# Performance work log

Measured on AMD Instinct MI355X. Metric: run time of the kernel, lower is better.

Reference implementation:

```python
import jax, jax.numpy as jnp
import numpy as np

K_MASK = -2.3819763e+38
ROPE_THETA = 1000000
MROPE_SECTION = (24, 20, 20)
NORM_EPS = 1e-6


def rms_norm(x, w, eps=NORM_EPS):
    dtype = x.dtype
    x32 = x.astype(jnp.float32)
    rms_inv = jax.lax.rsqrt(jnp.mean(x32 * x32, axis=-1, keepdims=True) + eps)
    return w * (x32 * rms_inv).astype(dtype)


def apply_rope(inputs, positions, head_dim, rope_theta=ROPE_THETA, mrope_section=MROPE_SECTION):
    # positions: [3, B, T] (temporal, height, width); inputs: [B, T, heads, head_dim]
    fraction = 2 * jnp.arange(0, head_dim // 2, dtype=jnp.float32) / head_dim
    timescale = rope_theta ** fraction  # [head_dim//2]
    sinusoid = positions[:, :, :, None].astype(jnp.float32) / timescale  # [3,B,T,hd/2]
    freq = sinusoid[0]
    h_idx = jnp.arange(1, mrope_section[1] * 3, 3)
    w_idx = jnp.arange(2, mrope_section[2] * 3, 3)
    freq = freq.at[..., h_idx].set(sinusoid[1][..., h_idx])
    freq = freq.at[..., w_idx].set(sinusoid[2][..., w_idx])
    freq = freq[:, :, None, :]  # [B,T,1,hd/2]
    sin, cos = jnp.sin(freq), jnp.cos(freq)
    first, second = jnp.split(inputs, 2, axis=-1)
    out = jnp.concatenate([first * cos - second * sin, second * cos + first * sin], axis=-1)
    return out.astype(inputs.dtype)


def setup_inputs() -> dict:
    key = jax.random.key(0)
    ks = jax.random.split(key, 6)
    B, T, D, N, K, H = 2, 1024, 2560, 32, 8, 128
    x = jax.random.normal(ks[0], (B, T, D), dtype=jnp.float32)
    positions = jnp.broadcast_to(jnp.arange(T, dtype=jnp.int32), (3, B, T))
    attn_mask = jnp.tril(jnp.ones((T, T), dtype=bool))[None].repeat(B, axis=0)  # causal [B,T,T]
    wq = jax.random.normal(ks[1], (D, N, H), dtype=jnp.float32) * 0.02
    wk = jax.random.normal(ks[2], (D, K, H), dtype=jnp.float32) * 0.02
    wv = jax.random.normal(ks[3], (D, K, H), dtype=jnp.float32) * 0.02
    wo = jax.random.normal(ks[4], (N, H, D), dtype=jnp.float32) * 0.02
    q_norm_w = jnp.ones((H,), dtype=jnp.float32)
    k_norm_w = jnp.ones((H,), dtype=jnp.float32)
    return {"x": x, "positions": positions, "attn_mask": attn_mask, "wq": wq,
            "wk": wk, "wv": wv, "wo": wo, "q_norm_w": q_norm_w, "k_norm_w": k_norm_w}


def reference(x, positions, attn_mask, wq, wk, wv, wo, q_norm_w, k_norm_w):
    head_dim = wo.shape[1]
    scale = head_dim ** -0.5
    q = rms_norm(jnp.einsum('btd,dnh->btnh', x, wq), q_norm_w)
    k = rms_norm(jnp.einsum('bsd,dkh->bskh', x, wk), k_norm_w)
    v = jnp.einsum('bsd,dkh->bskh', x, wv)
    q = apply_rope(q, positions, head_dim)
    k = apply_rope(k, positions, head_dim)
    b, t, qh, d = q.shape
    _, s, kh, _ = k.shape
    q = q.reshape((b, t, kh, qh // kh, d))  # GQA grouping
    attn = jnp.einsum('bthgd,bshd->bhgts', q, k) * scale
    attn = attn.reshape((b, qh, t, s))
    attn = jnp.where(attn_mask[:, None, :, :], attn, K_MASK)
    attn = jax.nn.softmax(attn.astype(jnp.float32), axis=-1).astype(k.dtype)
    attn = attn.reshape((b, kh, qh // kh, t, s))
    qkv = jnp.einsum('bhgts,bshd->bthgd', attn, v).reshape((b, t, qh, d))
    return jnp.einsum('btnh,nhd->btd', qkv, wo)
```

## Files before the change

kernel.cpp:

```cpp
#include <hip/hip_runtime.h>
#include <hip/hip_bf16.h>

typedef __attribute__((ext_vector_type(8))) __bf16 bf8_t;
typedef __attribute__((ext_vector_type(4))) float f32x4;
typedef __attribute__((ext_vector_type(16))) float f32x16;

#define GLOAD16(gptr, lptr)                                                              \
  __builtin_amdgcn_global_load_lds((const __attribute__((address_space(1))) void*)(gptr), \
                                   (__attribute__((address_space(3))) void*)(lptr), 16, 0, 0)

__device__ __forceinline__ unsigned short f2bf(float f) {
  union { float f; unsigned u; } v; v.f = f;
  return (unsigned short)((v.u + 0x7fffu + ((v.u >> 16) & 1u)) >> 16);
}

__device__ __forceinline__ float bf2f(unsigned short u) {
  union { unsigned u; float f; } v; v.u = ((unsigned)u) << 16;
  return v.f;
}

__device__ __forceinline__ unsigned cvtpk_bf16(float a, float b) {
  unsigned r;
  asm("v_cvt_pk_bf16_f32 %0, %1, %2" : "=v"(r) : "v"(a), "v"(b));
  return r;
}

__global__ void cast_bf16(const float* __restrict__ in, unsigned short* __restrict__ out, int n4) {
  int i = blockIdx.x * blockDim.x + threadIdx.x;
  if (i >= n4) return;
  float4 v = ((const float4*)in)[i];
  ushort4 o;
  o.x = f2bf(v.x); o.y = f2bf(v.y); o.z = f2bf(v.z); o.w = f2bf(v.w);
  ((ushort4*)out)[i] = o;
}

__global__ void tcast(const float* __restrict__ in, unsigned short* __restrict__ out,
                      int R, int C, int ld, int rowOff) {
  __shared__ float tile[32][33];
  int c0 = blockIdx.x * 32, r0 = blockIdx.y * 32;
  int tx = threadIdx.x, ty = threadIdx.y;
#pragma unroll
  for (int i = 0; i < 4; ++i)
    tile[ty + 8 * i][tx] = in[(size_t)(r0 + ty + 8 * i) * C + c0 + tx];
  __syncthreads();
#pragma unroll
  for (int i = 0; i < 4; ++i)
    out[(size_t)(rowOff + c0 + ty + 8 * i) * ld + r0 + tx] = f2bf(tile[tx][ty + 8 * i]);
}

__global__ __launch_bounds__(512, 2) void gemm256(
    const unsigned short* __restrict__ A,
    const unsigned short* __restrict__ Bt,
    float* __restrict__ C0, float* __restrict__ C1,
    unsigned short* __restrict__ Cb,
    int N, int ldk, int Kslice, int nTileN) {
  __shared__ unsigned short SM[4][2][8192];
  int ks = blockIdx.y;
  int kbase = ks * Kslice;
  int nwg = gridDim.x;
  int bidx = blockIdx.x;
  int wg = ((bidx & 7) * (nwg >> 3)) + (bidx >> 3);
  int bm = wg / nTileN, bn = wg % nTileN;
  int m0 = bm << 8, n0 = bn << 8;
  int tid = threadIdx.x, lane = tid & 63, w = tid >> 6;
  int wm = w >> 2, wn = w & 3;
  int lrow = lane & 15, lch = lane >> 4;
  int srow = tid >> 2;
  int scol = ((tid & 3) ^ ((srow >> 1) & 3)) << 3;
  int nt = Kslice >> 5;

  f32x4 acc[8][4] = {};

  auto stage = [&](int t) {
    int buf = t & 3;
    int k0 = kbase + (t << 5);
    const unsigned short* Ag = A + (size_t)(m0 + srow) * ldk + k0 + scol;
    const unsigned short* Bg = Bt + (size_t)(n0 + srow) * ldk + k0 + scol;
    unsigned short* Al = &SM[buf][0][w << 9];
    unsigned short* Bl = &SM[buf][1][w << 9];
    GLOAD16(Ag, Al);
    GLOAD16(Ag + (size_t)128 * ldk, Al + 4096);
    GLOAD16(Bg, Bl);
    GLOAD16(Bg + (size_t)128 * ldk, Bl + 4096);
  };

  stage(0);
  stage(1);
  stage(2);
  for (int t = 0; t < nt; ++t) {
    if (t + 2 < nt)      asm volatile("s_waitcnt vmcnt(8)" ::: "memory");
    else if (t + 1 < nt) asm volatile("s_waitcnt vmcnt(4)" ::: "memory");
    else                 asm volatile("s_waitcnt vmcnt(0)" ::: "memory");
    asm volatile("s_barrier" ::: "memory");
    if (t + 3 < nt) stage(t + 3);
    int buf = t & 3;
    const unsigned short* As = &SM[buf][0][0];
    const unsigned short* Bs = &SM[buf][1][0];
    bf8_t a[8], b[4];
#pragma unroll
    for (int mi = 0; mi < 8; ++mi) {
      int ar = (wm << 7) + (mi << 4) + lrow;
      a[mi] = *(const bf8_t*)(As + ar * 32 + ((lch ^ ((ar >> 1) & 3)) << 3));
    }
#pragma unroll
    for (int ni = 0; ni < 4; ++ni) {
      int br = (wn << 6) + (ni << 4) + lrow;
      b[ni] = *(const bf8_t*)(Bs + br * 32 + ((lch ^ ((br >> 1) & 3)) << 3));
    }
    __builtin_amdgcn_s_setprio(1);
#pragma unroll
    for (int mi = 0; mi < 8; ++mi)
#pragma unroll
      for (int ni = 0; ni < 4; ++ni)
        acc[mi][ni] = __builtin_amdgcn_mfma_f32_16x16x32_bf16(a[mi], b[ni], acc[mi][ni], 0, 0, 0);
    __builtin_amdgcn_s_setprio(0);
  }
  int r0 = m0 + (wm << 7) + (lch << 2);
  int c0 = n0 + (wn << 6) + lrow;
  if (Cb) {
#pragma unroll
    for (int mi = 0; mi < 8; ++mi)
#pragma unroll
      for (int ni = 0; ni < 4; ++ni)
#pragma unroll
        for (int r = 0; r < 4; ++r)
          Cb[(size_t)(r0 + (mi << 4) + r) * N + c0 + (ni << 4)] = f2bf(acc[mi][ni][r]);
  } else {
    float* __restrict__ C = ks ? C1 : C0;
#pragma unroll
    for (int mi = 0; mi < 8; ++mi)
#pragma unroll
      for (int ni = 0; ni < 4; ++ni)
#pragma unroll
        for (int r = 0; r < 4; ++r)
          C[(size_t)(r0 + (mi << 4) + r) * N + c0 + (ni << 4)] = acc[mi][ni][r];
  }
}

__global__ void reduce_add(const float4* __restrict__ a, const float4* __restrict__ b,
                           float4* __restrict__ o, int n4) {
  int i = blockIdx.x * blockDim.x + threadIdx.x;
  if (i >= n4) return;
  float4 x = a[i], y = b[i];
  o[i] = make_float4(x.x + y.x, x.y + y.y, x.z + y.z, x.w + y.w);
}

__global__ __launch_bounds__(128) void normrope(
    const unsigned short* __restrict__ qkv, const int* __restrict__ positions,
    const float* __restrict__ qw, const float* __restrict__ kw,
    unsigned short* __restrict__ qb, unsigned short* __restrict__ kb,
    unsigned short* __restrict__ vt) {
  int blk = blockIdx.x;
  int hh = blk % 48, bt = blk / 48;
  int b = bt >> 10, t = bt & 1023;
  int tid = threadIdx.x;
  int colbase = (hh < 32) ? (hh << 7) : ((hh < 40) ? (4096 + ((hh - 32) << 7)) : (5120 + ((hh - 40) << 7)));
  float val = bf2f(qkv[(size_t)bt * 6144 + colbase + tid]);
  if (hh >= 40) {
    vt[((size_t)((b * 8 + hh - 40) * 128 + tid)) * 1024 + t] = f2bf(val);
    return;
  }
  __shared__ float red[2];
  __shared__ float xs[128];
  float ss = val * val;
#pragma unroll
  for (int m = 32; m >= 1; m >>= 1) ss += __shfl_xor(ss, m);
  if ((tid & 63) == 0) red[tid >> 6] = ss;
  __syncthreads();
  float rinv = rsqrtf((red[0] + red[1]) * (1.0f / 128.0f) + 1e-6f);
  float wgt = (hh < 32) ? qw[tid] : kw[tid];
  float xn = val * rinv * wgt;
  xs[tid] = xn;
  __syncthreads();
  float other = xs[tid ^ 64];
  int pos = positions[b * 1024 + t];
  int j = tid & 63;
  float ang = (float)pos * exp2f(-(float)j * 0.31143075889569027f);
  float sv = sinf(ang), cv = cosf(ang);
  float outv = (tid < 64) ? (xn * cv - other * sv) : (xn * cv + other * sv);
  if (hh >= 32) outv *= 0.12751744f;
  unsigned short o = f2bf(outv);
  if (hh < 32) qb[((size_t)((b * 32 + hh) * 1024 + t)) * 128 + tid] = o;
  else kb[((size_t)((b * 8 + hh - 32) * 1024 + t)) * 128 + tid] = o;
}

__global__ __launch_bounds__(256, 2) void attn(
    const unsigned short* __restrict__ qb,
    const unsigned short* __restrict__ kb,
    const unsigned short* __restrict__ vt,
    unsigned short* __restrict__ ob) {
  __shared__ unsigned short Kl[2][64 * 128];
  __shared__ unsigned short Vl[2][128 * 64];
  int bx = blockIdx.x, hq = blockIdx.y, b = blockIdx.z;
  int qt = (bx < 4) ? (7 - bx) : (bx - 4);
  int kvh = hq >> 2;
  int tid = threadIdx.x, lane = tid & 63, w = tid >> 6;
  int qlane = lane & 31, h = lane >> 5;
  int q0 = (qt << 7) + (w << 5);
  int qg = q0 + qlane;
  const unsigned short* kbase = kb + ((size_t)(b * 8 + kvh) << 17);
  const unsigned short* vbase = vt + ((size_t)(b * 8 + kvh) << 17);

  const unsigned short* qptr = qb + ((size_t)((b * 32 + hq) * 1024 + qg) << 7) + (h << 3);
  bf8_t qf[8];
#pragma unroll
  for (int ds = 0; ds < 8; ++ds) qf[ds] = *(const bf8_t*)(qptr + ds * 16);

  f32x16 o[4] = {};
  float mrun = -3.0e38f, lrun = 0.f;
  int last_st = (q0 + 31) >> 6;
  int nsteps = 2 * qt + 2;

  auto stage = [&](int st, int buf) {
    int s0 = st << 6;
    unsigned short* kd = &Kl[buf][0];
    unsigned short* vd = &Vl[buf][0];
#pragma unroll
    for (int i = 0; i < 4; ++i) {
      int cid = i * 256 + tid;
      int kr = cid >> 4, ksl = cid & 15;
      GLOAD16(kbase + (size_t)(s0 + kr) * 128 + ((ksl ^ (kr & 15)) << 3), kd + cid * 8);
      int vr = cid >> 3, vsl = cid & 7;
      GLOAD16(vbase + (size_t)vr * 1024 + s0 + ((vsl ^ (vr & 7)) << 3), vd + cid * 8);
    }
  };

  stage(0, 0);
  for (int st = 0; st < nsteps; ++st) {
    __syncthreads();
    if (st + 1 < nsteps) stage(st + 1, (st + 1) & 1);
    if (st <= last_st) {
      const char* Kb = (const char*)&Kl[st & 1][0];
      const char* Vb = (const char*)&Vl[st & 1][0];
      f32x16 s0v = {}, s1v = {};
      __builtin_amdgcn_s_setprio(1);
#pragma unroll
      for (int ds = 0; ds < 8; ++ds) {
        int c = ds * 2 + h;
        int r0 = qlane, r1 = 32 + qlane;
        bf8_t k0 = *(const bf8_t*)(Kb + r0 * 256 + ((c ^ (r0 & 15)) << 4));
        bf8_t k1 = *(const bf8_t*)(Kb + r1 * 256 + ((c ^ (r1 & 15)) << 4));
        s0v = __builtin_amdgcn_mfma_f32_32x32x16_bf16(k0, qf[ds], s0v, 0, 0, 0);
        s1v = __builtin_amdgcn_mfma_f32_32x32x16_bf16(k1, qf[ds], s1v, 0, 0, 0);
      }
      __builtin_amdgcn_s_setprio(0);
      bool dm = (st == last_st);
      int kg0 = st << 6;
      float mt = -3.0e38f;
#pragma unroll
      for (int e = 0; e < 16; ++e) {
        int kl = (e & 3) + 8 * (e >> 2) + 4 * h;
        if (dm) {
          if (kg0 + kl > qg) s0v[e] = -3.0e38f;
          if (kg0 + 32 + kl > qg) s1v[e] = -3.0e38f;
        }
        mt = fmaxf(mt, fmaxf(s0v[e], s1v[e]));
      }
      mt = fmaxf(mt, __shfl_xor(mt, 32));
      if (!__all(mt - mrun <= 8.0f)) {
        float mnew = fmaxf(mrun, mt);
        float alpha = exp2f(mrun - mnew);
        lrun *= alpha;
#pragma unroll
        for (int db = 0; db < 4; ++db)
#pragma unroll
          for (int e = 0; e < 16; ++e) o[db][e] *= alpha;
        mrun = mnew;
      }
      float ls = 0.f;
#pragma unroll
      for (int e = 0; e < 16; ++e) {
        s0v[e] = exp2f(s0v[e] - mrun);
        s1v[e] = exp2f(s1v[e] - mrun);
        ls += s0v[e] + s1v[e];
      }
      ls += __shfl_xor(ls, 32);
      lrun += ls;
      bf8_t pf[4];
#pragma unroll
      for (int s = 0; s < 4; ++s) {
        unsigned w00, w01, w10, w11;
        {
          const int B0 = 4 * ((2 * s) & 3);
          if ((2 * s) >> 2) { w00 = cvtpk_bf16(s1v[B0], s1v[B0 + 1]); w01 = cvtpk_bf16(s1v[B0 + 2], s1v[B0 + 3]); }
          else              { w00 = cvtpk_bf16(s0v[B0], s0v[B0 + 1]); w01 = cvtpk_bf16(s0v[B0 + 2], s0v[B0 + 3]); }
        }
        {
          const int B1 = 4 * ((2 * s + 1) & 3);
          if ((2 * s + 1) >> 2) { w10 = cvtpk_bf16(s1v[B1], s1v[B1 + 1]); w11 = cvtpk_bf16(s1v[B1 + 2], s1v[B1 + 3]); }
          else                  { w10 = cvtpk_bf16(s0v[B1], s0v[B1 + 1]); w11 = cvtpk_bf16(s0v[B1 + 2], s0v[B1 + 3]); }
        }
        unsigned sa = h ? w00 : w10, sb = h ? w01 : w11;
        unsigned ra = __shfl_xor(sa, 32), rb = __shfl_xor(sb, 32);
        unsigned ka = h ? w10 : w00, kb2 = h ? w11 : w01;
        unsigned f0 = h ? ra : ka, f1 = h ? rb : kb2;
        unsigned f2 = h ? ka : ra, f3 = h ? kb2 : rb;
        uint4 fv = make_uint4(f0, f1, f2, f3);
        pf[s] = *(bf8_t*)&fv;
      }
      __builtin_amdgcn_s_setprio(1);
#pragma unroll
      for (int db = 0; db < 4; ++db) {
        int vr = (db << 5) + qlane;
#pragma unroll
        for (int s = 0; s < 4; ++s) {
          int c = (s << 1) + h;
          bf8_t vf = *(const bf8_t*)(Vb + vr * 128 + ((c ^ (vr & 7)) << 4));
          o[db] = __builtin_amdgcn_mfma_f32_32x32x16_bf16(vf, pf[s], o[db], 0, 0, 0);
        }
      }
      __builtin_amdgcn_s_setprio(0);
    }
  }

  __syncthreads();
  unsigned short* tb = &Kl[0][0] + (w << 12);
  float inv = 1.0f / lrun;
#pragma unroll
  for (int db = 0; db < 4; ++db)
#pragma unroll
    for (int rq = 0; rq < 4; ++rq) {
      int d0 = (db << 5) + (rq << 3) + (h << 2);
      unsigned lo = ((unsigned)f2bf(o[db][rq * 4 + 1] * inv) << 16) | f2bf(o[db][rq * 4 + 0] * inv);
      unsigned hi = ((unsigned)f2bf(o[db][rq * 4 + 3] * inv) << 16) | f2bf(o[db][rq * 4 + 2] * inv);
      *(uint2*)(tb + qlane * 128 + (d0 ^ ((qlane & 15) << 3))) = make_uint2(lo, hi);
    }
  int rr = lane >> 1, dh = (lane & 1) << 6;
  size_t orow = ((size_t)(b * 1024 + q0 + rr) << 12) + (hq << 7);
#pragma unroll
  for (int i = 0; i < 8; ++i) {
    int d8 = dh + i * 8;
    uint4 vv = *(const uint4*)(tb + rr * 128 + (d8 ^ ((rr & 15) << 3)));
    *(uint4*)(&ob[orow + d8]) = vv;
  }
}

extern "C" void kernel_launch(void* const* d_in, const int* in_sizes, int n_in,
                              void* d_out, int out_size, void* d_ws, size_t ws_size,
                              hipStream_t stream) {
  const float* x = (const float*)d_in[0];
  const int* positions = (const int*)d_in[1];
  const float* wq = (const float*)d_in[3];
  const float* wk = (const float*)d_in[4];
  const float* wv = (const float*)d_in[5];
  const float* wo = (const float*)d_in[6];
  const float* qnw = (const float*)d_in[7];
  const float* knw = (const float*)d_in[8];
  float* out = (float*)d_out;

  char* ws = (char*)d_ws;
  unsigned short* x_bf  = (unsigned short*)(ws);
  unsigned short* wqkvT = (unsigned short*)(ws + 10485760);
  unsigned short* woT   = (unsigned short*)(ws + 41943040);
  unsigned short* qkvb  = (unsigned short*)(ws + 62914560);
  float*          p0    = (float*)(ws + 62914560);
  float*          p1    = (float*)(ws + 83886080);
  unsigned short* q_bf  = (unsigned short*)(ws + 113246208);
  unsigned short* k_bf  = (unsigned short*)(ws + 130023424);
  unsigned short* vt_bf = (unsigned short*)(ws + 134217728);
  unsigned short* a_bf  = (unsigned short*)(ws + 138412032);

  cast_bf16<<<5120, 256, 0, stream>>>(x, x_bf, 2048 * 2560 / 4);
  tcast<<<dim3(128, 80), dim3(32, 8), 0, stream>>>(wq, wqkvT, 2560, 4096, 2560, 0);
  tcast<<<dim3(32, 80), dim3(32, 8), 0, stream>>>(wk, wqkvT, 2560, 1024, 2560, 4096);
  tcast<<<dim3(32, 80), dim3(32, 8), 0, stream>>>(wv, wqkvT, 2560, 1024, 2560, 5120);
  tcast<<<dim3(80, 128), dim3(32, 8), 0, stream>>>(wo, woT, 4096, 2560, 4096, 0);
  gemm256<<<dim3(8 * 24, 1), 512, 0, stream>>>(x_bf, wqkvT, nullptr, nullptr, qkvb,
                                               6144, 2560, 2560, 24);
  normrope<<<2048 * 48, 128, 0, stream>>>(qkvb, positions, qnw, knw, q_bf, k_bf, vt_bf);
  attn<<<dim3(8, 32, 2), 256, 0, stream>>>(q_bf, k_bf, vt_bf, a_bf);
  gemm256<<<dim3(8 * 10, 2), 512, 0, stream>>>(a_bf, woT, p0, p1, nullptr, 2560, 4096, 2048, 10);
  reduce_add<<<5120, 256, 0, stream>>>((const float4*)p0, (const float4*)p1, (float4*)out,
                                       2048 * 2560 / 4);
}
```

Measured before the change: 282.9 us.

## Split GEMM main loop into two half-tile MFMA phases with interleaved loads

The bf16 GEMM main loop is restructured so each K-step runs as two halves of the M fragments. The A and B global-to-LDS stages are issued separately, one before each MFMA half, and the LDS fragment reads for the second half and the next step are prefetched between MFMA phases. The goal is to overlap LDS reads and global loads with matrix-core work instead of loading all fragments before a single MFMA block. In exchange it adds several extra workgroup barriers per iteration and more fiddly vmcnt/lgkmcnt bookkeeping.

```diff
diff --git a/kernel.cpp b/kernel.cpp
--- a/kernel.cpp
+++ b/kernel.cpp
@@ -71,50 +71,84 @@
 
   f32x4 acc[8][4] = {};
 
-  auto stage = [&](int t) {
+  auto stageA = [&](int t) {
     int buf = t & 3;
     int k0 = kbase + (t << 5);
     const unsigned short* Ag = A + (size_t)(m0 + srow) * ldk + k0 + scol;
-    const unsigned short* Bg = Bt + (size_t)(n0 + srow) * ldk + k0 + scol;
     unsigned short* Al = &SM[buf][0][w << 9];
-    unsigned short* Bl = &SM[buf][1][w << 9];
     GLOAD16(Ag, Al);
     GLOAD16(Ag + (size_t)128 * ldk, Al + 4096);
+  };
+  auto stageB = [&](int t) {
+    int buf = t & 3;
+    int k0 = kbase + (t << 5);
+    const unsigned short* Bg = Bt + (size_t)(n0 + srow) * ldk + k0 + scol;
+    unsigned short* Bl = &SM[buf][1][w << 9];
     GLOAD16(Bg, Bl);
     GLOAD16(Bg + (size_t)128 * ldk, Bl + 4096);
   };
 
-  stage(0);
-  stage(1);
-  stage(2);
-  for (int t = 0; t < nt; ++t) {
-    if (t + 2 < nt)      asm volatile("s_waitcnt vmcnt(8)" ::: "memory");
-    else if (t + 1 < nt) asm volatile("s_waitcnt vmcnt(4)" ::: "memory");
-    else                 asm volatile("s_waitcnt vmcnt(0)" ::: "memory");
-    asm volatile("s_barrier" ::: "memory");
-    if (t + 3 < nt) stage(t + 3);
-    int buf = t & 3;
-    const unsigned short* As = &SM[buf][0][0];
-    const unsigned short* Bs = &SM[buf][1][0];
-    bf8_t a[8], b[4];
-#pragma unroll
-    for (int mi = 0; mi < 8; ++mi) {
-      int ar = (wm << 7) + (mi << 4) + lrow;
-      a[mi] = *(const bf8_t*)(As + ar * 32 + ((lch ^ ((ar >> 1) & 3)) << 3));
-    }
+  bf8_t bfr[4], afA[4], afB[4];
+  auto readBfr = [&](int t) {
+    const unsigned short* Bs = &SM[t & 3][1][0];
 #pragma unroll
     for (int ni = 0; ni < 4; ++ni) {
       int br = (wn << 6) + (ni << 4) + lrow;
-      b[ni] = *(const bf8_t*)(Bs + br * 32 + ((lch ^ ((br >> 1) & 3)) << 3));
-    }
+      bfr[ni] = *(const bf8_t*)(Bs + br * 32 + ((lch ^ ((br >> 1) & 3)) << 3));
+    }
+  };
+  auto readAfr = [&](int t, int half, bf8_t* af) {
+    const unsigned short* As = &SM[t & 3][0][0];
+#pragma unroll
+    for (int mi = 0; mi < 4; ++mi) {
+      int ar = (wm << 7) + ((half * 4 + mi) << 4) + lrow;
+      af[mi] = *(const bf8_t*)(As + ar * 32 + ((lch ^ ((ar >> 1) & 3)) << 3));
+    }
+  };
+
+  stageA(0); stageB(0); stageA(1); stageB(1); stageA(2); stageB(2);
+  asm volatile("s_waitcnt vmcnt(8)" ::: "memory");
+  asm volatile("s_barrier" ::: "memory");
+  readBfr(0);
+  readAfr(0, 0, afA);
+
+  for (int t = 0; t < nt; ++t) {
+    if (t + 3 < nt) stageA(t + 3);
+    asm volatile("s_barrier" ::: "memory");
+    asm volatile("s_waitcnt lgkmcnt(0)" ::: "memory");
+    __builtin_amdgcn_sched_barrier(0);
     __builtin_amdgcn_s_setprio(1);
 #pragma unroll
-    for (int mi = 0; mi < 8; ++mi)
+    for (int mi = 0; mi < 4; ++mi)
 #pragma unroll
       for (int ni = 0; ni < 4; ++ni)
-        acc[mi][ni] = __builtin_amdgcn_mfma_f32_16x16x32_bf16(a[mi], b[ni], acc[mi][ni], 0, 0, 0);
+        acc[mi][ni] = __builtin_amdgcn_mfma_f32_16x16x32_bf16(afA[mi], bfr[ni], acc[mi][ni], 0, 0, 0);
     __builtin_amdgcn_s_setprio(0);
+    asm volatile("s_barrier" ::: "memory");
+    readAfr(t, 1, afB);
+    if (t + 3 < nt) stageB(t + 3);
+    asm volatile("s_barrier" ::: "memory");
+    asm volatile("s_waitcnt lgkmcnt(0)" ::: "memory");
+    __builtin_amdgcn_sched_barrier(0);
+    __builtin_amdgcn_s_setprio(1);
+#pragma unroll
+    for (int mi = 0; mi < 4; ++mi)
+#pragma unroll
+      for (int ni = 0; ni < 4; ++ni)
+        acc[4 + mi][ni] = __builtin_amdgcn_mfma_f32_16x16x32_bf16(afB[mi], bfr[ni], acc[4 + mi][ni], 0, 0, 0);
+    __builtin_amdgcn_s_setprio(0);
+    if (t + 1 < nt) {
+      if (t + 3 < nt)      asm volatile("s_waitcnt vmcnt(8)" ::: "memory");
+      else if (t + 2 < nt) asm volatile("s_waitcnt vmcnt(4)" ::: "memory");
+      else                 asm volatile("s_waitcnt vmcnt(0)" ::: "memory");
+      asm volatile("s_barrier" ::: "memory");
+      readBfr(t + 1);
+      readAfr(t + 1, 0, afA);
+    } else {
+      asm volatile("s_barrier" ::: "memory");
+    }
   }
+
   int r0 = m0 + (wm << 7) + (lch << 2);
   int c0 = n0 + (wn << 6) + lrow;
   if (Cb) {
```

Result: slower. 294.2 us (+4.0%).
